# Kernel tuning notes

Hardware: AMD Instinct MI355X
Metric: run time of the kernel (lower is better)

The kernel has to match this reference:

```python
import jax, jax.numpy as jnp
import numpy as np

N_NODES = 100000
N_EDGES = 1600000
IN_DIM, HID_DIM, OUT_DIM = 128, 64, 64
NEG_SLOPE = 0.2


def _gat_layer(h_in, src, dst, W, a_src, a_dst, b, n_nodes):
    # h: [N, F_out]
    h = h_in @ W.T
    alpha_src = h @ a_src  # [N]
    alpha_dst = h @ a_dst  # [N]
    # per-edge raw attention logits (edge j->i: src=j, dst=i)
    e = jax.nn.leaky_relu(alpha_src[src] + alpha_dst[dst], NEG_SLOPE)  # [E]
    # segment softmax over incoming edges of each dst node
    m = jax.ops.segment_max(e, dst, num_segments=n_nodes)
    ex = jnp.exp(e - m[dst])
    denom = jax.ops.segment_sum(ex, dst, num_segments=n_nodes)
    alpha = ex / denom[dst]  # [E], denom > 0 thanks to self-loops
    out = jax.ops.segment_sum(h[src] * alpha[:, None], dst, num_segments=n_nodes)
    return out + b


def setup_inputs() -> dict:
    key = jax.random.key(0)
    ks = jax.random.split(key, 12)
    x = jax.random.normal(ks[0], (N_NODES, IN_DIM), dtype=jnp.float32)
    edge_index = jax.random.randint(ks[1], (2, N_EDGES), 0, N_NODES)
    edge_attr = jax.random.normal(ks[2], (N_EDGES, 1), dtype=jnp.float32)
    s1 = 1.0 / np.sqrt(IN_DIM)
    s2 = 1.0 / np.sqrt(HID_DIM)
    W1 = jax.random.normal(ks[3], (HID_DIM, IN_DIM), dtype=jnp.float32) * s1
    att_src1 = jax.random.normal(ks[4], (HID_DIM,), dtype=jnp.float32) * s2
    att_dst1 = jax.random.normal(ks[5], (HID_DIM,), dtype=jnp.float32) * s2
    b1 = jnp.zeros((HID_DIM,), dtype=jnp.float32)
    W2 = jax.random.normal(ks[6], (OUT_DIM, HID_DIM), dtype=jnp.float32) * s2
    att_src2 = jax.random.normal(ks[7], (OUT_DIM,), dtype=jnp.float32) * s2
    att_dst2 = jax.random.normal(ks[8], (OUT_DIM,), dtype=jnp.float32) * s2
    b2 = jnp.zeros((OUT_DIM,), dtype=jnp.float32)
    return {"x": x, "edge_index": edge_index, "edge_attr": edge_attr,
            "W1": W1, "att_src1": att_src1, "att_dst1": att_dst1, "b1": b1,
            "W2": W2, "att_src2": att_src2, "att_dst2": att_dst2, "b2": b2}


def reference(x, edge_index, edge_attr, W1, att_src1, att_dst1, b1,
              W2, att_src2, att_dst2, b2):
    n = x.shape[0]
    # add self-loops (PyG GATConv default); edge_attr unused (edge_dim=None)
    loop = jnp.arange(n, dtype=edge_index.dtype)
    src = jnp.concatenate([edge_index[0], loop])
    dst = jnp.concatenate([edge_index[1], loop])
    h = _gat_layer(x, src, dst, W1, att_src1, att_dst1, b1, n)
    h = jax.nn.relu(h)
    h = _gat_layer(h, src, dst, W2, att_src2, att_dst2, b2, n)
    # global_mean_pool with batch=None -> mean over all nodes, shape [1, F]
    return jnp.mean(h, axis=0, keepdims=True)
```

## Files before the change

kernel.cpp:

```cpp
#include <hip/hip_runtime.h>

#define NEG_SLOPE 0.2f
#define BSHIFT 6
#define NBMAX 2048
#define BCAP 1408
#define ESTRIDE (BCAP + 64)
#define CHUNK 4096

typedef __attribute__((ext_vector_type(8))) short short8;
typedef __attribute__((ext_vector_type(4))) float f32x4;

__device__ __forceinline__ unsigned short f2b(float x) {
    unsigned u = __float_as_uint(x);
    u += 0x7fff + ((u >> 16) & 1);
    return (unsigned short)(u >> 16);
}
__device__ __forceinline__ float b2f(unsigned short u) {
    return __uint_as_float((unsigned)u << 16);
}

__global__ __launch_bounds__(256) void hist_kernel(
    const int* __restrict__ ei, int* __restrict__ hist, int E, int NB)
{
    __shared__ int cnt[NBMAX];
    const int tid = threadIdx.x;
    for (int i = tid; i < NB; i += 256) cnt[i] = 0;
    __syncthreads();
    const int start = blockIdx.x * CHUNK;
    const int end = min(start + CHUNK, E);
    for (int i = start + tid; i < end; i += 256)
        atomicAdd(&cnt[ei[E + i] >> BSHIFT], 1);
    __syncthreads();
    for (int i = tid; i < NB; i += 256)
        hist[(size_t)blockIdx.x * NB + i] = cnt[i];
}

__global__ __launch_bounds__(256) void colscan_kernel(
    int* __restrict__ hist, int* __restrict__ btotal, int NB, int NBLK)
{
    const int col = (int)((blockIdx.x * 256 + threadIdx.x) >> 6);
    const int ln  = threadIdx.x & 63;
    if (col >= NB) return;
    int run = 0;
    for (int r0 = 0; r0 < NBLK; r0 += 64) {
        const int r = r0 + ln;
        const bool ok = (r < NBLK);
        int v = ok ? hist[(size_t)r * NB + col] : 0;
        int inc = v;
        #pragma unroll
        for (int off = 1; off < 64; off <<= 1) {
            int x = __shfl_up(inc, off, 64);
            if (ln >= off) inc += x;
        }
        if (ok) hist[(size_t)r * NB + col] = run + inc - v;
        run += __shfl(inc, 63, 64);
    }
    if (ln == 0) btotal[col] = run;
}

template<int K, bool BF16IN>
__device__ __forceinline__ void gemm_attn_core(
    unsigned short* __restrict__ xb, unsigned short* __restrict__ wb,
    float* __restrict__ avs, float* __restrict__ avd, int bid,
    const void* __restrict__ in_v, const float* __restrict__ W,
    const float* __restrict__ a_src, const float* __restrict__ a_dst,
    unsigned short* __restrict__ hb, float* __restrict__ asrc,
    float* __restrict__ adst, int N)
{
    constexpr int LDK = K + 8;
    const int tid = threadIdx.x;
    const int node0 = bid * 64;
    const int w = tid >> 6;
    const int lane = tid & 63;
    const int col = lane & 15;
    const int quad = lane >> 4;

    if (tid < 64) { avs[tid] = a_src[tid]; avd[tid] = a_dst[tid]; }

    for (int i = tid; i < 64 * (K / 4); i += 256) {
        int r = i / (K / 4), c = i % (K / 4);
        float4 v = *(const float4*)&W[(size_t)r * K + 4 * c];
        *(ushort4*)&wb[r * LDK + 4 * c] =
            make_ushort4(f2b(v.x), f2b(v.y), f2b(v.z), f2b(v.w));
    }
    if (BF16IN) {
        const unsigned short* in = (const unsigned short*)in_v;
        for (int i = tid; i < 64 * (K / 8); i += 256) {
            int r = i / (K / 8), c = i % (K / 8);
            int node = node0 + r;
            ulonglong2 v = (node < N)
                ? *(const ulonglong2*)&in[(size_t)node * K + 8 * c]
                : make_ulonglong2(0ull, 0ull);
            *(ulonglong2*)&xb[r * LDK + 8 * c] = v;
        }
    } else {
        const float* in = (const float*)in_v;
        for (int i = tid; i < 64 * (K / 4); i += 256) {
            int r = i / (K / 4), c = i % (K / 4);
            int node = node0 + r;
            float4 v = (node < N) ? *(const float4*)&in[(size_t)node * K + 4 * c]
                                  : make_float4(0.f, 0.f, 0.f, 0.f);
            *(ushort4*)&xb[r * LDK + 4 * c] =
                make_ushort4(f2b(v.x), f2b(v.y), f2b(v.z), f2b(v.w));
        }
    }
    __syncthreads();

    f32x4 acc[4] = {f32x4{0,0,0,0}, f32x4{0,0,0,0}, f32x4{0,0,0,0}, f32x4{0,0,0,0}};
    #pragma unroll
    for (int kc = 0; kc < K / 32; ++kc) {
        short8 a = *(const short8*)&xb[(16 * w + col) * LDK + kc * 32 + quad * 8];
        #pragma unroll
        for (int j = 0; j < 4; ++j) {
            short8 b = *(const short8*)&wb[(16 * j + col) * LDK + kc * 32 + quad * 8];
            acc[j] = __builtin_amdgcn_mfma_f32_16x16x32_bf16(a, b, acc[j], 0, 0, 0);
        }
    }

    #pragma unroll
    for (int r = 0; r < 4; ++r) {
        const int node = node0 + 16 * w + quad * 4 + r;
        const bool valid = node < N;
        float vs = 0.f, vd = 0.f;
        #pragma unroll
        for (int j = 0; j < 4; ++j) {
            float hv = acc[j][r];
            int f = 16 * j + col;
            if (valid) hb[(size_t)node * 64 + f] = f2b(hv);
            vs = fmaf(hv, avs[f], vs);
            vd = fmaf(hv, avd[f], vd);
        }
        #pragma unroll
        for (int off = 8; off >= 1; off >>= 1) {
            vs += __shfl_down(vs, off, 16);
            vd += __shfl_down(vd, off, 16);
        }
        if (col == 0 && valid) { asrc[node] = vs; adst[node] = vd; }
    }
}

__global__ __launch_bounds__(256) void scatter_gemm_kernel(
    const int* __restrict__ ei, const int* __restrict__ hist,
    int* __restrict__ binned, int E, int NB, int nblk,
    const float* __restrict__ x, const float* __restrict__ W1,
    const float* __restrict__ as1, const float* __restrict__ ad1,
    unsigned short* __restrict__ hb, float* __restrict__ asrc,
    float* __restrict__ adst, int N)
{
    extern __shared__ char smem[];
    if ((int)blockIdx.x < nblk) {
        int* base = (int*)smem;
        int* cnt2 = base + NBMAX;
        const int q = nblk >> 3, rr = nblk & 7;
        const int xs = blockIdx.x & 7, k = blockIdx.x >> 3;
        const int chunk = ((xs < rr) ? xs * (q + 1) : rr * (q + 1) + (xs - rr) * q) + k;
        const int tid = threadIdx.x;
        for (int i = tid; i < NB; i += 256) {
            base[i] = hist[(size_t)chunk * NB + i];
            cnt2[i] = 0;
        }
        __syncthreads();
        const int start = chunk * CHUNK;
        const int end = min(start + CHUNK, E);
        for (int i = start + tid; i < end; i += 256) {
            int s = ei[i], d = ei[E + i];
            int b = d >> BSHIFT;
            int r = base[b] + atomicAdd(&cnt2[b], 1);
            if (r < BCAP) binned[(size_t)b * BCAP + r] = (s << BSHIFT) | (d & 63);
        }
    } else {
        constexpr int LDK = 128 + 8;
        unsigned short* xb = (unsigned short*)smem;
        unsigned short* wb = xb + 64 * LDK;
        float* avs = (float*)(wb + 64 * LDK);
        float* avd = avs + 64;
        gemm_attn_core<128, false>(xb, wb, avs, avd, (int)blockIdx.x - nblk,
                                   x, W1, as1, ad1, hb, asrc, adst, N);
    }
}

__global__ __launch_bounds__(256) void bucket_csr_kernel(
    const int* __restrict__ binned, const int* __restrict__ btotal,
    int* __restrict__ row_ptr, int* __restrict__ rend,
    int* __restrict__ esrc, int N)
{
    __shared__ int ldeg[64];
    __shared__ int lcur[64];
    const int b = blockIdx.x;
    const int tid = threadIdx.x;
    const int node0 = b << BSHIFT;
    const int cnt = min(btotal[b], BCAP);
    const int base_e = b * ESTRIDE;
    const int* bp = binned + (size_t)b * BCAP;

    if (tid < 64) ldeg[tid] = (node0 + tid < N) ? 1 : 0;
    __syncthreads();
    for (int i = tid; i < cnt; i += 256)
        atomicAdd(&ldeg[bp[i] & 63], 1);
    __syncthreads();
    if (tid < 64) {
        int v = ldeg[tid];
        int inc = v;
        #pragma unroll
        for (int off = 1; off < 64; off <<= 1) {
            int t2 = __shfl_up(inc, off, 64);
            if (tid >= off) inc += t2;
        }
        int excl = inc - v;
        int node = node0 + tid;
        if (node < N) {
            row_ptr[node] = base_e + excl;
            rend[node] = base_e + excl + v;
            esrc[base_e + excl] = node;
            lcur[tid] = base_e + excl + 1;
        }
    }
    __syncthreads();
    for (int i = tid; i < cnt; i += 256) {
        int v = bp[i];
        int pos = atomicAdd(&lcur[v & 63], 1);
        esrc[pos] = v >> BSHIFT;
    }
}

template<int K, bool BF16IN>
__global__ __launch_bounds__(256) void gemm_attn_kernel(
    const void* __restrict__ in_v, const float* __restrict__ W,
    const float* __restrict__ a_src, const float* __restrict__ a_dst,
    unsigned short* __restrict__ hb, float* __restrict__ asrc,
    float* __restrict__ adst, int N)
{
    constexpr int LDK = K + 8;
    __shared__ unsigned short xb[64 * LDK];
    __shared__ unsigned short wb[64 * LDK];
    __shared__ float avs[64], avd[64];
    gemm_attn_core<K, BF16IN>(xb, wb, avs, avd, (int)blockIdx.x,
                              in_v, W, a_src, a_dst, hb, asrc, adst, N);
}

__global__ __launch_bounds__(256) void aggregate_csr_kernel(
    const int* __restrict__ row_ptr, const int* __restrict__ rend,
    const int* __restrict__ esrc,
    const float* __restrict__ asrc, const float* __restrict__ adst,
    const unsigned short* __restrict__ hb, const float* __restrict__ bias,
    unsigned short* __restrict__ gb, int N, int do_relu)
{
    const int node = (int)((blockIdx.x * 256 + threadIdx.x) >> 4);
    const int lane = threadIdx.x & 15;
    if (node >= N) return;
    const int beg = row_ptr[node];
    const int end = rend[node];
    const float ad = adst[node];
    float a0 = 0.f, a1 = 0.f, a2 = 0.f, a3 = 0.f, wsum = 0.f;
    int p = beg;
    for (; p + 4 <= end; p += 4) {
        int s[4]; ushort4 r[4]; float l[4];
        #pragma unroll
        for (int j = 0; j < 4; ++j) s[j] = esrc[p + j];
        #pragma unroll
        for (int j = 0; j < 4; ++j)
            r[j] = *(const ushort4*)(hb + (size_t)s[j] * 64 + lane * 4);
        #pragma unroll
        for (int j = 0; j < 4; ++j) l[j] = asrc[s[j]] + ad;
        #pragma unroll
        for (int j = 0; j < 4; ++j) {
            float ll = (l[j] > 0.f) ? l[j] : NEG_SLOPE * l[j];
            float w = __expf(ll);
            wsum += w;
            a0 = fmaf(w, b2f(r[j].x), a0);
            a1 = fmaf(w, b2f(r[j].y), a1);
            a2 = fmaf(w, b2f(r[j].z), a2);
            a3 = fmaf(w, b2f(r[j].w), a3);
        }
    }
    for (; p < end; ++p) {
        int s = esrc[p];
        ushort4 r = *(const ushort4*)(hb + (size_t)s * 64 + lane * 4);
        float l = asrc[s] + ad;
        l = (l > 0.f) ? l : NEG_SLOPE * l;
        float w = __expf(l);
        wsum += w;
        a0 = fmaf(w, b2f(r.x), a0);
        a1 = fmaf(w, b2f(r.y), a1);
        a2 = fmaf(w, b2f(r.z), a2);
        a3 = fmaf(w, b2f(r.w), a3);
    }
    const float inv = 1.0f / wsum;
    float4 v = make_float4(a0 * inv, a1 * inv, a2 * inv, a3 * inv);
    if (bias) {
        v.x += bias[lane * 4 + 0]; v.y += bias[lane * 4 + 1];
        v.z += bias[lane * 4 + 2]; v.w += bias[lane * 4 + 3];
    }
    if (do_relu) {
        v.x = fmaxf(v.x, 0.f); v.y = fmaxf(v.y, 0.f);
        v.z = fmaxf(v.z, 0.f); v.w = fmaxf(v.w, 0.f);
    }
    *(ushort4*)&gb[(size_t)node * 64 + lane * 4] =
        make_ushort4(f2b(v.x), f2b(v.y), f2b(v.z), f2b(v.w));
}

__global__ __launch_bounds__(256) void pool_kernel(
    const unsigned short* __restrict__ gb, const float* __restrict__ b2,
    float* __restrict__ out, int N)
{
    __shared__ float red[256];
    const int f = threadIdx.x & 63;
    const int sub = threadIdx.x >> 6;
    float acc = 0.f;
    for (int n = blockIdx.x * 4 + sub; n < N; n += gridDim.x * 4)
        acc += b2f(gb[(size_t)n * 64 + f]);
    red[threadIdx.x] = acc;
    __syncthreads();
    if (threadIdx.x < 64) {
        float s = red[f] + red[64 + f] + red[128 + f] + red[192 + f];
        atomicAdd(out + f, s * (1.0f / (float)N));
        if (blockIdx.x == 0) atomicAdd(out + f, b2[f]);
    }
}

extern "C" void kernel_launch(void* const* d_in, const int* in_sizes, int n_in,
                              void* d_out, int out_size, void* d_ws, size_t ws_size,
                              hipStream_t stream) {
    const float* x   = (const float*)d_in[0];
    const int*   ei  = (const int*)d_in[1];
    const float* W1  = (const float*)d_in[3];
    const float* as1 = (const float*)d_in[4];
    const float* ad1 = (const float*)d_in[5];
    const float* b1  = (const float*)d_in[6];
    const float* W2  = (const float*)d_in[7];
    const float* as2 = (const float*)d_in[8];
    const float* ad2 = (const float*)d_in[9];
    const float* b2  = (const float*)d_in[10];
    float* out = (float*)d_out;

    const int N = in_sizes[0] / 128;
    const int E = in_sizes[1] / 2;
    const int NB = (N + 63) >> BSHIFT;
    const int NBLK = (E + CHUNK - 1) / CHUNK;

    auto align4 = [](size_t v) { return (v + 3) & ~(size_t)3; };
    float* ws    = (float*)d_ws;
    size_t off = 0;
    unsigned short* hb = (unsigned short*)(ws + off); off += align4((size_t)N * 32);
    unsigned short* gb = (unsigned short*)(ws + off); off += align4((size_t)N * 32);
    float* asrc  = ws + off; off += align4(N);
    float* adst  = ws + off; off += align4(N);
    int* row_ptr = (int*)(ws + off); off += align4(N);
    int* rend    = (int*)(ws + off); off += align4(N);
    int* btotal  = (int*)(ws + off); off += NBMAX;
    int* hist    = (int*)(ws + off); off += align4((size_t)NBLK * NB);
    int* esrc    = (int*)(ws + off); off += align4((size_t)NB * ESTRIDE);
    int* binned  = (int*)gb;

    const int gemm_blocks = (N + 63) / 64;
    const int agg_blocks  = (int)(((size_t)N * 16 + 255) / 256);
    const int packed_lds  = 64 * (128 + 8) * 2 * 2 + 2 * 64 * 4;

    hipMemsetAsync(out, 0, 64 * sizeof(float), stream);

    hist_kernel<<<NBLK, 256, 0, stream>>>(ei, hist, E, NB);
    colscan_kernel<<<(NB * 64 + 255) / 256, 256, 0, stream>>>(hist, btotal, NB, NBLK);
    scatter_gemm_kernel<<<NBLK + gemm_blocks, 256, packed_lds, stream>>>(
        ei, hist, binned, E, NB, NBLK, x, W1, as1, ad1, hb, asrc, adst, N);
    bucket_csr_kernel<<<NB, 256, 0, stream>>>(binned, btotal, row_ptr, rend, esrc, N);

    aggregate_csr_kernel<<<agg_blocks, 256, 0, stream>>>(
        row_ptr, rend, esrc, asrc, adst, hb, b1, gb, N, 1);

    gemm_attn_kernel<64, true><<<gemm_blocks, 256, 0, stream>>>(
        gb, W2, as2, ad2, hb, asrc, adst, N);
    aggregate_csr_kernel<<<agg_blocks, 256, 0, stream>>>(
        row_ptr, rend, esrc, asrc, adst, hb, nullptr, gb, N, 0);

    pool_kernel<<<512, 256, 0, stream>>>(gb, b2, out, N);
}
```

Measured before the change: 271.1 us.

## Replace histogram+scan with atomic bucket reservation and fuse pooling into aggregation

Removes the separate histogram and column-scan kernels. Each scatter block now counts its bucket occupancy in registers and shared memory, then reserves a range per bucket with a global atomicAdd on a bucket cursor, so the edge indices are read only once. The second-layer aggregation also reduces its per-node outputs into per-block partial sums, which removes the bf16 output write and the full re-read for pooling. In exchange, edge order inside a bucket is no longer deterministic, and bucket_csr now receives the final cursor values as totals.

```diff
diff --git a/kernel.cpp b/kernel.cpp
--- a/kernel.cpp
+++ b/kernel.cpp
@@ -17,45 +17,6 @@
 }
 __device__ __forceinline__ float b2f(unsigned short u) {
     return __uint_as_float((unsigned)u << 16);
-}
-
-__global__ __launch_bounds__(256) void hist_kernel(
-    const int* __restrict__ ei, int* __restrict__ hist, int E, int NB)
-{
-    __shared__ int cnt[NBMAX];
-    const int tid = threadIdx.x;
-    for (int i = tid; i < NB; i += 256) cnt[i] = 0;
-    __syncthreads();
-    const int start = blockIdx.x * CHUNK;
-    const int end = min(start + CHUNK, E);
-    for (int i = start + tid; i < end; i += 256)
-        atomicAdd(&cnt[ei[E + i] >> BSHIFT], 1);
-    __syncthreads();
-    for (int i = tid; i < NB; i += 256)
-        hist[(size_t)blockIdx.x * NB + i] = cnt[i];
-}
-
-__global__ __launch_bounds__(256) void colscan_kernel(
-    int* __restrict__ hist, int* __restrict__ btotal, int NB, int NBLK)
-{
-    const int col = (int)((blockIdx.x * 256 + threadIdx.x) >> 6);
-    const int ln  = threadIdx.x & 63;
-    if (col >= NB) return;
-    int run = 0;
-    for (int r0 = 0; r0 < NBLK; r0 += 64) {
-        const int r = r0 + ln;
-        const bool ok = (r < NBLK);
-        int v = ok ? hist[(size_t)r * NB + col] : 0;
-        int inc = v;
-        #pragma unroll
-        for (int off = 1; off < 64; off <<= 1) {
-            int x = __shfl_up(inc, off, 64);
-            if (ln >= off) inc += x;
-        }
-        if (ok) hist[(size_t)r * NB + col] = run + inc - v;
-        run += __shfl(inc, 63, 64);
-    }
-    if (ln == 0) btotal[col] = run;
 }
 
 template<int K, bool BF16IN>
@@ -139,8 +100,8 @@
     }
 }
 
-__global__ __launch_bounds__(256) void scatter_gemm_kernel(
-    const int* __restrict__ ei, const int* __restrict__ hist,
+__global__ __launch_bounds__(256) void build_gemm_kernel(
+    const int* __restrict__ ei, int* __restrict__ bcur,
     int* __restrict__ binned, int E, int NB, int nblk,
     const float* __restrict__ x, const float* __restrict__ W1,
     const float* __restrict__ as1, const float* __restrict__ ad1,
@@ -149,24 +110,42 @@
 {
     extern __shared__ char smem[];
     if ((int)blockIdx.x < nblk) {
-        int* base = (int*)smem;
-        int* cnt2 = base + NBMAX;
+        int* cnt  = (int*)smem;
+        int* base = cnt + NBMAX;
         const int q = nblk >> 3, rr = nblk & 7;
         const int xs = blockIdx.x & 7, k = blockIdx.x >> 3;
         const int chunk = ((xs < rr) ? xs * (q + 1) : rr * (q + 1) + (xs - rr) * q) + k;
         const int tid = threadIdx.x;
-        for (int i = tid; i < NB; i += 256) {
-            base[i] = hist[(size_t)chunk * NB + i];
-            cnt2[i] = 0;
-        }
+
+        for (int i = tid; i < NB; i += 256) cnt[i] = 0;
         __syncthreads();
+
         const int start = chunk * CHUNK;
         const int end = min(start + CHUNK, E);
-        for (int i = start + tid; i < end; i += 256) {
-            int s = ei[i], d = ei[E + i];
-            int b = d >> BSHIFT;
-            int r = base[b] + atomicAdd(&cnt2[b], 1);
-            if (r < BCAP) binned[(size_t)b * BCAP + r] = (s << BSHIFT) | (d & 63);
+        int sv[16], dv[16];
+        #pragma unroll
+        for (int j = 0; j < 16; ++j) {
+            int i = start + tid + j * 256;
+            bool ok = i < end;
+            sv[j] = ok ? ei[i] : 0;
+            dv[j] = ok ? ei[E + i] : -1;
+            if (ok) atomicAdd(&cnt[dv[j] >> BSHIFT], 1);
+        }
+        __syncthreads();
+        for (int i = tid; i < NB; i += 256) {
+            int c = cnt[i];
+            base[i] = c ? atomicAdd(&bcur[i], c) : 0;
+            cnt[i] = 0;
+        }
+        __syncthreads();
+        #pragma unroll
+        for (int j = 0; j < 16; ++j) {
+            if (dv[j] >= 0) {
+                int b = dv[j] >> BSHIFT;
+                int r = base[b] + atomicAdd(&cnt[b], 1);
+                if (r < BCAP)
+                    binned[(size_t)b * BCAP + r] = (sv[j] << BSHIFT) | (dv[j] & 63);
+            }
         }
     } else {
         constexpr int LDK = 128 + 8;
@@ -299,16 +278,80 @@
         make_ushort4(f2b(v.x), f2b(v.y), f2b(v.z), f2b(v.w));
 }
 
-__global__ __launch_bounds__(256) void pool_kernel(
-    const unsigned short* __restrict__ gb, const float* __restrict__ b2,
-    float* __restrict__ out, int N)
+__global__ __launch_bounds__(256) void aggregate_pool2_kernel(
+    const int* __restrict__ row_ptr, const int* __restrict__ rend,
+    const int* __restrict__ esrc,
+    const float* __restrict__ asrc, const float* __restrict__ adst,
+    const unsigned short* __restrict__ hb, float* __restrict__ partial, int N)
+{
+    __shared__ float red[64];
+    const int tid = threadIdx.x;
+    if (tid < 64) red[tid] = 0.f;
+    __syncthreads();
+
+    const int node = (int)((blockIdx.x * 256 + tid) >> 4);
+    const int lane = tid & 15;
+    const bool valid = node < N;
+    const int beg = valid ? row_ptr[node] : 0;
+    const int end = valid ? rend[node] : 0;
+    const float ad = valid ? adst[node] : 0.f;
+
+    float a0 = 0.f, a1 = 0.f, a2 = 0.f, a3 = 0.f, wsum = 0.f;
+    int p = beg;
+    for (; p + 4 <= end; p += 4) {
+        int s[4]; ushort4 r[4]; float l[4];
+        #pragma unroll
+        for (int j = 0; j < 4; ++j) s[j] = esrc[p + j];
+        #pragma unroll
+        for (int j = 0; j < 4; ++j)
+            r[j] = *(const ushort4*)(hb + (size_t)s[j] * 64 + lane * 4);
+        #pragma unroll
+        for (int j = 0; j < 4; ++j) l[j] = asrc[s[j]] + ad;
+        #pragma unroll
+        for (int j = 0; j < 4; ++j) {
+            float ll = (l[j] > 0.f) ? l[j] : NEG_SLOPE * l[j];
+            float w = __expf(ll);
+            wsum += w;
+            a0 = fmaf(w, b2f(r[j].x), a0);
+            a1 = fmaf(w, b2f(r[j].y), a1);
+            a2 = fmaf(w, b2f(r[j].z), a2);
+            a3 = fmaf(w, b2f(r[j].w), a3);
+        }
+    }
+    for (; p < end; ++p) {
+        int s = esrc[p];
+        ushort4 r = *(const ushort4*)(hb + (size_t)s * 64 + lane * 4);
+        float l = asrc[s] + ad;
+        l = (l > 0.f) ? l : NEG_SLOPE * l;
+        float w = __expf(l);
+        wsum += w;
+        a0 = fmaf(w, b2f(r.x), a0);
+        a1 = fmaf(w, b2f(r.y), a1);
+        a2 = fmaf(w, b2f(r.z), a2);
+        a3 = fmaf(w, b2f(r.w), a3);
+    }
+
+    if (valid) {
+        const float inv = 1.0f / wsum;
+        atomicAdd(&red[lane * 4 + 0], a0 * inv);
+        atomicAdd(&red[lane * 4 + 1], a1 * inv);
+        atomicAdd(&red[lane * 4 + 2], a2 * inv);
+        atomicAdd(&red[lane * 4 + 3], a3 * inv);
+    }
+    __syncthreads();
+    if (tid < 64) partial[(size_t)blockIdx.x * 64 + tid] = red[tid];
+}
+
+__global__ __launch_bounds__(256) void pool_reduce_kernel(
+    const float* __restrict__ partial, const float* __restrict__ b2,
+    float* __restrict__ out, int nrows, int N)
 {
     __shared__ float red[256];
     const int f = threadIdx.x & 63;
     const int sub = threadIdx.x >> 6;
     float acc = 0.f;
-    for (int n = blockIdx.x * 4 + sub; n < N; n += gridDim.x * 4)
-        acc += b2f(gb[(size_t)n * 64 + f]);
+    for (int n = blockIdx.x * 4 + sub; n < nrows; n += gridDim.x * 4)
+        acc += partial[(size_t)n * 64 + f];
     red[threadIdx.x] = acc;
     __syncthreads();
     if (threadIdx.x < 64) {
@@ -347,30 +390,30 @@
     float* adst  = ws + off; off += align4(N);
     int* row_ptr = (int*)(ws + off); off += align4(N);
     int* rend    = (int*)(ws + off); off += align4(N);
-    int* btotal  = (int*)(ws + off); off += NBMAX;
-    int* hist    = (int*)(ws + off); off += align4((size_t)NBLK * NB);
+    int* bcur    = (int*)(ws + off); off += NBMAX;
+    float* partial = ws + off;
+    const int agg_blocks  = (int)(((size_t)N * 16 + 255) / 256);
+    off += align4((size_t)agg_blocks * 64);
     int* esrc    = (int*)(ws + off); off += align4((size_t)NB * ESTRIDE);
     int* binned  = (int*)gb;
 
     const int gemm_blocks = (N + 63) / 64;
-    const int agg_blocks  = (int)(((size_t)N * 16 + 255) / 256);
     const int packed_lds  = 64 * (128 + 8) * 2 * 2 + 2 * 64 * 4;
 
     hipMemsetAsync(out, 0, 64 * sizeof(float), stream);
-
-    hist_kernel<<<NBLK, 256, 0, stream>>>(ei, hist, E, NB);
-    colscan_kernel<<<(NB * 64 + 255) / 256, 256, 0, stream>>>(hist, btotal, NB, NBLK);
-    scatter_gemm_kernel<<<NBLK + gemm_blocks, 256, packed_lds, stream>>>(
-        ei, hist, binned, E, NB, NBLK, x, W1, as1, ad1, hb, asrc, adst, N);
-    bucket_csr_kernel<<<NB, 256, 0, stream>>>(binned, btotal, row_ptr, rend, esrc, N);
+    hipMemsetAsync(bcur, 0, NBMAX * sizeof(int), stream);
+
+    build_gemm_kernel<<<NBLK + gemm_blocks, 256, packed_lds, stream>>>(
+        ei, bcur, binned, E, NB, NBLK, x, W1, as1, ad1, hb, asrc, adst, N);
+    bucket_csr_kernel<<<NB, 256, 0, stream>>>(binned, bcur, row_ptr, rend, esrc, N);
 
     aggregate_csr_kernel<<<agg_blocks, 256, 0, stream>>>(
         row_ptr, rend, esrc, asrc, adst, hb, b1, gb, N, 1);
 
     gemm_attn_kernel<64, true><<<gemm_blocks, 256, 0, stream>>>(
         gb, W2, as2, ad2, hb, asrc, adst, N);
-    aggregate_csr_kernel<<<agg_blocks, 256, 0, stream>>>(
-        row_ptr, rend, esrc, asrc, adst, hb, nullptr, gb, N, 0);
-
-    pool_kernel<<<512, 256, 0, stream>>>(gb, b2, out, N);
-}
+    aggregate_pool2_kernel<<<agg_blocks, 256, 0, stream>>>(
+        row_ptr, rend, esrc, asrc, adst, hb, partial, N);
+
+    pool_reduce_kernel<<<512, 256, 0, stream>>>(partial, b2, out, agg_blocks, N);
+}
```

After: 287.9 us. 1.06x slower.

## Replace histogram and column scan with global atomic bucket reservation

Applied to the files above, without the earlier changes.

Removes the separate histogram and column-scan kernels. Each scatter block now builds a local bucket histogram from register-held edges, reserves space in each bucket with a global atomicAdd on a per-bucket cursor, and then scatters into it. This saves two kernel launches and the round trip of the NBLK×NB histogram through memory. In exchange, edges within a bucket land in nondeterministic order and the global cursors see contention from concurrent blocks.

```diff
diff --git a/kernel.cpp b/kernel.cpp
--- a/kernel.cpp
+++ b/kernel.cpp
@@ -17,45 +17,6 @@
 }
 __device__ __forceinline__ float b2f(unsigned short u) {
     return __uint_as_float((unsigned)u << 16);
-}
-
-__global__ __launch_bounds__(256) void hist_kernel(
-    const int* __restrict__ ei, int* __restrict__ hist, int E, int NB)
-{
-    __shared__ int cnt[NBMAX];
-    const int tid = threadIdx.x;
-    for (int i = tid; i < NB; i += 256) cnt[i] = 0;
-    __syncthreads();
-    const int start = blockIdx.x * CHUNK;
-    const int end = min(start + CHUNK, E);
-    for (int i = start + tid; i < end; i += 256)
-        atomicAdd(&cnt[ei[E + i] >> BSHIFT], 1);
-    __syncthreads();
-    for (int i = tid; i < NB; i += 256)
-        hist[(size_t)blockIdx.x * NB + i] = cnt[i];
-}
-
-__global__ __launch_bounds__(256) void colscan_kernel(
-    int* __restrict__ hist, int* __restrict__ btotal, int NB, int NBLK)
-{
-    const int col = (int)((blockIdx.x * 256 + threadIdx.x) >> 6);
-    const int ln  = threadIdx.x & 63;
-    if (col >= NB) return;
-    int run = 0;
-    for (int r0 = 0; r0 < NBLK; r0 += 64) {
-        const int r = r0 + ln;
-        const bool ok = (r < NBLK);
-        int v = ok ? hist[(size_t)r * NB + col] : 0;
-        int inc = v;
-        #pragma unroll
-        for (int off = 1; off < 64; off <<= 1) {
-            int x = __shfl_up(inc, off, 64);
-            if (ln >= off) inc += x;
-        }
-        if (ok) hist[(size_t)r * NB + col] = run + inc - v;
-        run += __shfl(inc, 63, 64);
-    }
-    if (ln == 0) btotal[col] = run;
 }
 
 template<int K, bool BF16IN>
@@ -139,8 +100,8 @@
     }
 }
 
-__global__ __launch_bounds__(256) void scatter_gemm_kernel(
-    const int* __restrict__ ei, const int* __restrict__ hist,
+__global__ __launch_bounds__(256) void build_gemm_kernel(
+    const int* __restrict__ ei, int* __restrict__ bcur,
     int* __restrict__ binned, int E, int NB, int nblk,
     const float* __restrict__ x, const float* __restrict__ W1,
     const float* __restrict__ as1, const float* __restrict__ ad1,
@@ -149,24 +110,42 @@
 {
     extern __shared__ char smem[];
     if ((int)blockIdx.x < nblk) {
-        int* base = (int*)smem;
-        int* cnt2 = base + NBMAX;
+        int* cnt  = (int*)smem;
+        int* base = cnt + NBMAX;
         const int q = nblk >> 3, rr = nblk & 7;
         const int xs = blockIdx.x & 7, k = blockIdx.x >> 3;
         const int chunk = ((xs < rr) ? xs * (q + 1) : rr * (q + 1) + (xs - rr) * q) + k;
         const int tid = threadIdx.x;
-        for (int i = tid; i < NB; i += 256) {
-            base[i] = hist[(size_t)chunk * NB + i];
-            cnt2[i] = 0;
-        }
+
+        for (int i = tid; i < NB; i += 256) cnt[i] = 0;
         __syncthreads();
+
         const int start = chunk * CHUNK;
         const int end = min(start + CHUNK, E);
-        for (int i = start + tid; i < end; i += 256) {
-            int s = ei[i], d = ei[E + i];
-            int b = d >> BSHIFT;
-            int r = base[b] + atomicAdd(&cnt2[b], 1);
-            if (r < BCAP) binned[(size_t)b * BCAP + r] = (s << BSHIFT) | (d & 63);
+        int sv[16], dv[16];
+        #pragma unroll
+        for (int j = 0; j < 16; ++j) {
+            int i = start + tid + j * 256;
+            bool ok = i < end;
+            sv[j] = ok ? ei[i] : 0;
+            dv[j] = ok ? ei[E + i] : -1;
+            if (ok) atomicAdd(&cnt[dv[j] >> BSHIFT], 1);
+        }
+        __syncthreads();
+        for (int i = tid; i < NB; i += 256) {
+            int c = cnt[i];
+            base[i] = c ? atomicAdd(&bcur[i], c) : 0;
+            cnt[i] = 0;
+        }
+        __syncthreads();
+        #pragma unroll
+        for (int j = 0; j < 16; ++j) {
+            if (dv[j] >= 0) {
+                int b = dv[j] >> BSHIFT;
+                int r = base[b] + atomicAdd(&cnt[b], 1);
+                if (r < BCAP)
+                    binned[(size_t)b * BCAP + r] = (sv[j] << BSHIFT) | (dv[j] & 63);
+            }
         }
     } else {
         constexpr int LDK = 128 + 8;
@@ -347,8 +326,7 @@
     float* adst  = ws + off; off += align4(N);
     int* row_ptr = (int*)(ws + off); off += align4(N);
     int* rend    = (int*)(ws + off); off += align4(N);
-    int* btotal  = (int*)(ws + off); off += NBMAX;
-    int* hist    = (int*)(ws + off); off += align4((size_t)NBLK * NB);
+    int* bcur    = (int*)(ws + off); off += NBMAX;
     int* esrc    = (int*)(ws + off); off += align4((size_t)NB * ESTRIDE);
     int* binned  = (int*)gb;
 
@@ -357,12 +335,11 @@
     const int packed_lds  = 64 * (128 + 8) * 2 * 2 + 2 * 64 * 4;
 
     hipMemsetAsync(out, 0, 64 * sizeof(float), stream);
-
-    hist_kernel<<<NBLK, 256, 0, stream>>>(ei, hist, E, NB);
-    colscan_kernel<<<(NB * 64 + 255) / 256, 256, 0, stream>>>(hist, btotal, NB, NBLK);
-    scatter_gemm_kernel<<<NBLK + gemm_blocks, 256, packed_lds, stream>>>(
-        ei, hist, binned, E, NB, NBLK, x, W1, as1, ad1, hb, asrc, adst, N);
-    bucket_csr_kernel<<<NB, 256, 0, stream>>>(binned, btotal, row_ptr, rend, esrc, N);
+    hipMemsetAsync(bcur, 0, NBMAX * sizeof(int), stream);
+
+    build_gemm_kernel<<<NBLK + gemm_blocks, 256, packed_lds, stream>>>(
+        ei, bcur, binned, E, NB, NBLK, x, W1, as1, ad1, hb, asrc, adst, N);
+    bucket_csr_kernel<<<NB, 256, 0, stream>>>(binned, bcur, row_ptr, rend, esrc, N);
 
     aggregate_csr_kernel<<<agg_blocks, 256, 0, stream>>>(
         row_ptr, rend, esrc, asrc, adst, hb, b1, gb, N, 1);
```

New measurement: 272.2 us. About the same (+0.4%).
